# Performance work log

Hardware: AMD Instinct MI355X
Metric: run time of the kernel (lower is better)

The kernel has to match this reference:

```python
import jax, jax.numpy as jnp
import numpy as np


def _rel_index(h):
    # static relative-position index for an h x h grid (torch meshgrid 'ij')
    coords = np.stack(np.meshgrid(np.arange(h), np.arange(h), indexing='ij'))  # (2,h,h)
    cf = coords.reshape(2, -1)                       # (2, N)
    rel = cf[:, :, None] - cf[:, None, :]            # (2, N, N)
    rel = rel.transpose(1, 2, 0)                     # (N, N, 2)
    rel[..., 0] += h - 1
    rel[..., 1] += h - 1
    rel[..., 0] *= 2 * h - 1
    return rel.sum(-1)                               # (N, N) int


def _conv2d_s2(x, w, b):
    y = jax.lax.conv_general_dilated(x, w, window_strides=(2, 2),
                                     padding=[(1, 1), (1, 1)],
                                     dimension_numbers=('NCHW', 'OIHW', 'NCHW'))
    return y + b[None, :, None, None]


def _attn(z, qkv_w, qkv_b, out_w, out_b, table, heads):
    # H == reduce_size for every layer in this config, so no interp of K/V.
    B, C, H, W = z.shape
    N = H * W
    inner = qkv_w.shape[0] // 3
    d = inner // heads
    qkv = jnp.einsum('oc,bchw->bohw', qkv_w, z) + qkv_b[None, :, None, None]
    q, k, v = jnp.split(qkv, 3, axis=1)
    # channel layout is (dim_head, heads) with heads fastest (einops '(dim_head heads)')
    def split_heads(t):
        return t.reshape(B, d, heads, N).transpose(0, 2, 3, 1)  # b h n d
    q, k, v = split_heads(q), split_heads(k), split_heads(v)
    att = jnp.einsum('bhid,bhjd->bhij', q, k)
    idx = _rel_index(H)
    bias = table[idx.reshape(-1)].reshape(N, N, heads).transpose(2, 0, 1)  # (h, N, N)
    att = (att + bias[None]) * (d ** -0.5)  # bias added BEFORE scale, as in source
    att = jax.nn.softmax(att, axis=-1)
    o = jnp.einsum('bhij,bhjd->bhid', att, v)
    o = o.transpose(0, 3, 1, 2).reshape(B, d * heads, H, W)  # back to (dim_head heads) layout
    return jnp.einsum('oc,bchw->bohw', out_w, o) + out_b[None, :, None, None]


def setup_inputs() -> dict:
    key = jax.random.key(0)
    ks = jax.random.split(key, 24)
    heads = 3
    dims = [16, 32, 64]
    in_chs = [1, 16, 32]
    reds = [32, 16, 8]
    inp = {'x': jax.random.normal(ks[0], (32, 1, 64, 64), dtype=jnp.float32)}
    j = 1
    for i, (dim, cin, r) in enumerate(zip(dims, in_chs, reds), start=1):
        dh = dim // heads
        inner = dh * heads
        inp[f'conv{i}_w'] = jax.random.normal(ks[j], (dim, cin, 3, 3), dtype=jnp.float32) * 0.05; j += 1
        inp[f'conv{i}_b'] = jax.random.normal(ks[j], (dim,), dtype=jnp.float32) * 0.01; j += 1
        inp[f'qkv{i}_w'] = jax.random.normal(ks[j], (inner * 3, dim), dtype=jnp.float32) * 0.05; j += 1
        inp[f'qkv{i}_b'] = jax.random.normal(ks[j], (inner * 3,), dtype=jnp.float32) * 0.01; j += 1
        inp[f'out{i}_w'] = jax.random.normal(ks[j], (dim, inner), dtype=jnp.float32) * 0.05; j += 1
        inp[f'out{i}_b'] = jax.random.normal(ks[j], (dim,), dtype=jnp.float32) * 0.01; j += 1
        inp[f'rel{i}'] = jax.random.normal(ks[j], ((2 * r - 1) * (2 * r - 1), heads), dtype=jnp.float32) * 0.02; j += 1
    inp['cls_w'] = jax.random.normal(ks[j], (10, 64), dtype=jnp.float32) * 0.05; j += 1
    inp['cls_b'] = jax.random.normal(ks[j], (10,), dtype=jnp.float32) * 0.01
    return inp


def reference(x, conv1_w, conv1_b, qkv1_w, qkv1_b, out1_w, out1_b, rel1,
              conv2_w, conv2_b, qkv2_w, qkv2_b, out2_w, out2_b, rel2,
              conv3_w, conv3_b, qkv3_w, qkv3_b, out3_w, out3_b, rel3,
              cls_w, cls_b):
    heads = 3
    z = jax.nn.relu(_conv2d_s2(x, conv1_w, conv1_b))
    z = _attn(z, qkv1_w, qkv1_b, out1_w, out1_b, rel1, heads) + z
    z = jax.nn.relu(_conv2d_s2(z, conv2_w, conv2_b))
    z = _attn(z, qkv2_w, qkv2_b, out2_w, out2_b, rel2, heads) + z
    z = jax.nn.relu(_conv2d_s2(z, conv3_w, conv3_b))
    z = _attn(z, qkv3_w, qkv3_b, out3_w, out3_b, rel3, heads) + z
    z = z.mean(axis=(2, 3))           # adaptive avg pool to 1x1 + flatten -> (B, 64)
    cls_output = z @ cls_w.T + cls_b  # CLS_head linear (dropout inactive in eval)
    return (z, cls_output)
```

## Files before the change

kernel.cpp:

```cpp
#include <hip/hip_runtime.h>
#include <math.h>

#define CDIV(a, b) (((a) + (b) - 1) / (b))

#define LOG2E 1.4426950408889634f
#define SC5  (0.44721359549996f * LOG2E)
#define SC10 (0.31622776601684f * LOG2E)
#define SC21 (0.21821789023599f * LOG2E)
#define EXP2(x) __builtin_amdgcn_exp2f(x)

template <int CIN, int HIN, int COUT, int HOUT, int INNER, int DP, int KVRS, int KVD, int TPX>
__global__ void __launch_bounds__(256) conv_qkv(const float* __restrict__ in,
                                                const float* __restrict__ cw,
                                                const float* __restrict__ cb,
                                                const float* __restrict__ qw,
                                                const float* __restrict__ qb,
                                                float* __restrict__ z, float* __restrict__ q,
                                                float* __restrict__ kv) {
    constexpr int N = HOUT * HOUT;
    __shared__ float zt[COUT * TPX];
    const int b  = blockIdx.x / (N / TPX);
    const int n0 = (blockIdx.x % (N / TPX)) * TPX;
    const int tid = threadIdx.x;

    for (int idx = tid; idx < COUT * TPX; idx += 256) {
        int c = idx / TPX, px = idx % TPX;
        int n = n0 + px;
        int ho = n / HOUT, wo = n % HOUT;
        float acc = cb[c];
        for (int ci = 0; ci < CIN; ++ci) {
            const float* ip = in + (size_t)(b * CIN + ci) * HIN * HIN;
            const float* wp = cw + (size_t)(c * CIN + ci) * 9;
            #pragma unroll
            for (int kh = 0; kh < 3; ++kh) {
                int hi = 2 * ho + kh - 1;
                if (hi < 0 || hi >= HIN) continue;
                #pragma unroll
                for (int kw = 0; kw < 3; ++kw) {
                    int wi = 2 * wo + kw - 1;
                    if (wi < 0 || wi >= HIN) continue;
                    acc = fmaf(wp[kh * 3 + kw], ip[hi * HIN + wi], acc);
                }
            }
        }
        acc = fmaxf(acc, 0.f);
        zt[idx] = acc;
        z[((size_t)(b * COUT) + c) * N + n] = acc;
    }
    __syncthreads();

    constexpr int OC3 = 3 * INNER;
    for (int idx = tid; idx < OC3 * TPX; idx += 256) {
        int oc = idx / TPX, px = idx % TPX;
        float val = qb[oc];
        const float* wp = qw + (size_t)oc * COUT;
        #pragma unroll 8
        for (int c = 0; c < COUT; ++c) val = fmaf(wp[c], zt[c * TPX + px], val);
        int part = oc / INNER;
        int r = oc - part * INNER;
        int hh = r % 3, dd = r / 3;
        size_t n = n0 + px;
        if (part == 0)
            q[((size_t)(b * 3 + hh) * N + n) * DP + dd] = val;
        else
            kv[((size_t)(b * 3 + hh) * N + n) * KVRS + (part - 1) * KVD + dd] = val;
    }
}

template <int CPREV, int INNERP, int DPREV, int HINW, int COUT, int HOUT, int INNER, int DP,
          int KVRS, int KVD, int TPX>
__global__ void __launch_bounds__(256) fused_oc(const float* __restrict__ o1,
                                                const float* __restrict__ ow,
                                                const float* __restrict__ ob,
                                                const float* __restrict__ zres,
                                                const float* __restrict__ cw,
                                                const float* __restrict__ cb,
                                                const float* __restrict__ qw,
                                                const float* __restrict__ qb,
                                                float* __restrict__ z, float* __restrict__ q,
                                                float* __restrict__ kv) {
    constexpr int N2 = HOUT * HOUT;
    constexpr int N1 = HINW * HINW;
    constexpr int TROWS = TPX / HOUT;
    constexpr int HR = 2 * TROWS + 1;
    constexpr int HALO = HR * HINW;
    __shared__ float smem[INNERP * HALO + CPREV * HALO];
    float* o1s = smem;
    float* zh  = smem + INNERP * HALO;
    float* zt  = smem;
    const int b  = blockIdx.x / (N2 / TPX);
    const int n0 = (blockIdx.x % (N2 / TPX)) * TPX;
    const int tid = threadIdx.x;
    const int ho0 = n0 / HOUT;
    const int row0 = 2 * ho0 - 1;

    for (int t = tid; t < INNERP * HALO; t += 256) {
        int hd = t / HALO, p = t - hd * HALO;
        int row = row0 + p / HINW;
        float v = 0.f;
        if (row >= 0 && row < HINW)
            v = o1[((size_t)(b * INNERP + hd)) * N1 + row * HINW + (p % HINW)];
        o1s[t] = v;
    }
    __syncthreads();

    for (int t = tid; t < CPREV * HALO; t += 256) {
        int ci = t / HALO, p = t - ci * HALO;
        int row = row0 + p / HINW;
        float val = 0.f;
        if (row >= 0 && row < HINW) {
            int n1 = row * HINW + (p % HINW);
            val = ob[ci] + zres[((size_t)(b * CPREV) + ci) * N1 + n1];
            const float* wp = ow + (size_t)ci * INNERP;
            for (int dd = 0; dd < DPREV; ++dd) {
                #pragma unroll
                for (int hh = 0; hh < 3; ++hh)
                    val = fmaf(wp[dd * 3 + hh], o1s[(hh * DPREV + dd) * HALO + p], val);
            }
        }
        zh[t] = val;
    }
    __syncthreads();

    for (int idx = tid; idx < COUT * TPX; idx += 256) {
        int c = idx / TPX, px = idx - (idx / TPX) * TPX;
        int hol = px / HOUT, wo = px - hol * HOUT;
        float acc = cb[c];
        for (int ci = 0; ci < CPREV; ++ci) {
            const float* zp = zh + ci * HALO;
            const float* wp = cw + (size_t)(c * CPREV + ci) * 9;
            #pragma unroll
            for (int kh = 0; kh < 3; ++kh) {
                int r = 2 * hol + kh;
                #pragma unroll
                for (int kw = 0; kw < 3; ++kw) {
                    int col = 2 * wo + kw - 1;
                    if (col < 0 || col >= HINW) continue;
                    acc = fmaf(wp[kh * 3 + kw], zp[r * HINW + col], acc);
                }
            }
        }
        acc = fmaxf(acc, 0.f);
        zt[idx] = acc;
        z[((size_t)(b * COUT) + c) * N2 + n0 + px] = acc;
    }
    __syncthreads();

    constexpr int OC3 = 3 * INNER;
    for (int idx = tid; idx < OC3 * TPX; idx += 256) {
        int oc = idx / TPX, px = idx % TPX;
        float val = qb[oc];
        const float* wp = qw + (size_t)oc * COUT;
        #pragma unroll 8
        for (int c = 0; c < COUT; ++c) val = fmaf(wp[c], zt[c * TPX + px], val);
        int part = oc / INNER;
        int r = oc - part * INNER;
        int hh = r % 3, dd = r / 3;
        size_t n = n0 + px;
        if (part == 0)
            q[((size_t)(b * 3 + hh) * N2 + n) * DP + dd] = val;
        else
            kv[((size_t)(b * 3 + hh) * N2 + n) * KVRS + (part - 1) * KVD + dd] = val;
    }
}

template <int D, int QP, int RS, int RPT, int TILE, int NW>
__global__ void __launch_bounds__(NW * 64) attn_big(const float* __restrict__ q,
                                                    const float* __restrict__ kv,
                                                    const float* __restrict__ table,
                                                    float* __restrict__ o, int N, int log2Hg,
                                                    int T, float scale2) {
    extern __shared__ float smem[];
    float* tb = smem;
    float* comb = smem;
    constexpr int BT = NW * 64;
    constexpr int ROWS = 64 * RPT;
    constexpr int CSTR = (D % 2 == 0) ? (D + 3) : (D + 2);
    constexpr int RV4 = RS / 4;
    constexpr int NLD = (TILE * RV4 + 63) / 64;
    constexpr bool FULL = (TILE * RV4) % 64 == 0;

    const int bh = blockIdx.x % 96;
    const int chunk = blockIdx.x / 96;
    const int h = bh % 3;
    const int tid = threadIdx.x;
    const int wave = tid >> 6;
    const int lane = tid & 63;
    const int Hg = 1 << log2Hg;
    const int W2 = 2 * Hg - 1;
    const int base = chunk * ROWS;

    float* kvw = smem + ((T + 3) & ~3) + wave * (2 * TILE * RS);

    for (int t = tid; t < T; t += BT) tb[t] = table[t * 3 + h] * scale2;

    float qr[RPT][D];
    const float* tbp[RPT];
    #pragma unroll
    for (int r = 0; r < RPT; ++r) {
        int i = base + lane + 64 * r;
        const float* qg = q + ((size_t)bh * N + i) * QP;
        #pragma unroll
        for (int dd = 0; dd < D; ++dd) qr[r][dd] = qg[dd];
        tbp[r] = tb + (((i >> log2Hg) + Hg - 1) * W2 + (i & (Hg - 1)) + Hg - 1);
    }

    float acc[RPT][D];
    float lsum[RPT];
    #pragma unroll
    for (int r = 0; r < RPT; ++r) {
        lsum[r] = 0.f;
        #pragma unroll
        for (int dd = 0; dd < D; ++dd) acc[r][dd] = 0.f;
    }

    const float4* kvb4 = (const float4*)(kv + (size_t)bh * N * RS);
    const int NJ = N / NW;
    const int NT = NJ / TILE;
    const int j0 = wave * NJ;

    float4 sreg[NLD];
    {
        const float4* src = kvb4 + (size_t)j0 * RV4;
        #pragma unroll
        for (int x = 0; x < NLD; ++x) {
            int idx = lane + 64 * x;
            if (FULL || idx < TILE * RV4) sreg[x] = src[idx];
        }
        float4* dst4 = (float4*)kvw;
        #pragma unroll
        for (int x = 0; x < NLD; ++x) {
            int idx = lane + 64 * x;
            if (FULL || idx < TILE * RV4) dst4[idx] = sreg[x];
        }
    }

    __syncthreads();

    for (int t = 0; t < NT; ++t) {
        float* curb = kvw + (t & 1) * (TILE * RS);
        if (t + 1 < NT) {
            const float4* src = kvb4 + (size_t)(j0 + (t + 1) * TILE) * RV4;
            #pragma unroll
            for (int x = 0; x < NLD; ++x) {
                int idx = lane + 64 * x;
                if (FULL || idx < TILE * RV4) sreg[x] = src[idx];
            }
        }
        const int jt = j0 + t * TILE;
        for (int jg = 0; jg < TILE; jg += 4) {
            #pragma unroll
            for (int k = 0; k < 4; ++k) {
                const int j = jt + jg + k;
                const float* kr = curb + (jg + k) * RS;
                const int joff = (j >> log2Hg) * W2 + (j & (Hg - 1));
                #pragma unroll
                for (int r = 0; r < RPT; ++r) {
                    float s = 0.f;
                    #pragma unroll
                    for (int dd = 0; dd < D; ++dd) s = fmaf(qr[r][dd], kr[dd], s);
                    float e = EXP2(fmaf(s, scale2, tbp[r][-joff]));
                    lsum[r] += e;
                    #pragma unroll
                    for (int dd = 0; dd < D; ++dd) acc[r][dd] = fmaf(e, kr[D + dd], acc[r][dd]);
                }
            }
        }
        if (t + 1 < NT) {
            float4* dst4 = (float4*)(kvw + ((t + 1) & 1) * (TILE * RS));
            #pragma unroll
            for (int x = 0; x < NLD; ++x) {
                int idx = lane + 64 * x;
                if (FULL || idx < TILE * RV4) dst4[idx] = sreg[x];
            }
        }
    }

    __syncthreads();
    #pragma unroll
    for (int r = 0; r < RPT; ++r) {
        float* cp = comb + (size_t)(wave * ROWS + lane + 64 * r) * CSTR;
        #pragma unroll
        for (int dd = 0; dd < D; ++dd) cp[dd] = acc[r][dd];
        cp[D] = lsum[r];
    }
    __syncthreads();
    if (tid < ROWS) {
        float af[D];
        #pragma unroll
        for (int dd = 0; dd < D; ++dd) af[dd] = 0.f;
        float lf = 0.f;
        #pragma unroll
        for (int wv = 0; wv < NW; ++wv) {
            const float* cp = comb + (size_t)(wv * ROWS + tid) * CSTR;
            #pragma unroll
            for (int dd = 0; dd < D; ++dd) af[dd] += cp[dd];
            lf += cp[D];
        }
        float inv = 1.0f / lf;
        int i = base + tid;
        #pragma unroll
        for (int dd = 0; dd < D; ++dd)
            o[((size_t)bh * D + dd) * N + i] = af[dd] * inv;
    }
}

__global__ void __launch_bounds__(256) attn_small(const float* __restrict__ q,
                                                  const float* __restrict__ kv,
                                                  const float* __restrict__ table,
                                                  float* __restrict__ o, float scale2) {
    constexpr int D = 21, DP = 24, NN = 64;
    constexpr int CSTR = 23;
    __shared__ float smem[4 * NN * CSTR];
    float* kvs = smem;
    float* tb = kvs + NN * 2 * DP;
    float* comb = smem;

    const int bh = blockIdx.x;
    const int h = bh % 3;
    const int tid = threadIdx.x;
    const int wave = tid >> 6;
    const int lane = tid & 63;

    {
        const float4* kvg = (const float4*)(kv + (size_t)bh * NN * 2 * DP);
        float4* kvs4 = (float4*)kvs;
        for (int t = tid; t < NN * 2 * DP / 4; t += 256) kvs4[t] = kvg[t];
        for (int t = tid; t < 225; t += 256) tb[t] = table[t * 3 + h] * scale2;
    }

    const int i = lane;
    const float* qg = q + ((size_t)bh * NN + i) * DP;
    float qr[D];
    #pragma unroll
    for (int dd = 0; dd < D; ++dd) qr[dd] = qg[dd];
    const int ibase = ((i >> 3) + 7) * 15 + (i & 7) + 7;
    __syncthreads();

    float acc[D];
    #pragma unroll
    for (int dd = 0; dd < D; ++dd) acc[dd] = 0.f;
    float lsum = 0.f;

    const int j0 = wave * 16;
    #pragma unroll
    for (int jj = 0; jj < 16; ++jj) {
        const int j = j0 + jj;
        float4 r4[12];
        const float4* rp = (const float4*)(kvs + j * 2 * DP);
        #pragma unroll
        for (int x = 0; x < 12; ++x) r4[x] = rp[x];
        const float* kr = (const float*)r4;
        const float* vr = kr + DP;
        const int joff = (j >> 3) * 15 + (j & 7);
        float s = 0.f;
        #pragma unroll
        for (int dd = 0; dd < D; ++dd) s = fmaf(qr[dd], kr[dd], s);
        float e = EXP2(fmaf(s, scale2, tb[ibase - joff]));
        lsum += e;
        #pragma unroll
        for (int dd = 0; dd < D; ++dd) acc[dd] = fmaf(e, vr[dd], acc[dd]);
    }

    __syncthreads();
    {
        float* cp = comb + (size_t)(wave * NN + lane) * CSTR;
        #pragma unroll
        for (int dd = 0; dd < D; ++dd) cp[dd] = acc[dd];
        cp[D] = lsum;
    }
    __syncthreads();
    if (tid < NN) {
        float af[D];
        #pragma unroll
        for (int dd = 0; dd < D; ++dd) af[dd] = 0.f;
        float lf = 0.f;
        #pragma unroll
        for (int wv = 0; wv < 4; ++wv) {
            const float* cp = comb + (size_t)(wv * NN + tid) * CSTR;
            #pragma unroll
            for (int dd = 0; dd < D; ++dd) af[dd] += cp[dd];
            lf += cp[D];
        }
        float inv = 1.0f / lf;
        #pragma unroll
        for (int dd = 0; dd < D; ++dd)
            o[((size_t)bh * D + dd) * NN + tid] = af[dd] * inv;
    }
}

__global__ void __launch_bounds__(256) tail(const float* __restrict__ o,
                                            const float* __restrict__ ow,
                                            const float* __restrict__ ob,
                                            const float* __restrict__ zin,
                                            const float* __restrict__ cw,
                                            const float* __restrict__ cb,
                                            float* __restrict__ out) {
    __shared__ float os[63 * 64];
    __shared__ float zt[64 * 65];
    __shared__ float p[64];
    const int b = blockIdx.x;
    const int tid = threadIdx.x;
    for (int t = tid; t < 63 * 64; t += 256) os[t] = o[(size_t)(b * 63) * 64 + t];
    __syncthreads();
    for (int idx = tid; idx < 64 * 64; idx += 256) {
        int c = idx >> 6, n = idx & 63;
        float val = ob[c] + zin[((size_t)(b * 64) + c) * 64 + n];
        const float* wp = ow + (size_t)c * 63;
        for (int dd = 0; dd < 21; ++dd) {
            #pragma unroll
            for (int hh = 0; hh < 3; ++hh)
                val = fmaf(wp[dd * 3 + hh], os[(hh * 21 + dd) * 64 + n], val);
        }
        zt[c * 65 + n] = val;
    }
    __syncthreads();
    if (tid < 64) {
        float s = 0.f;
        #pragma unroll
        for (int n = 0; n < 64; ++n) s += zt[tid * 65 + n];
        s *= (1.0f / 64.0f);
        p[tid] = s;
        out[b * 64 + tid] = s;
    }
    __syncthreads();
    if (tid < 10) {
        float val = cb[tid];
        const float* wp = cw + (size_t)tid * 64;
        #pragma unroll
        for (int kk = 0; kk < 64; ++kk) val = fmaf(wp[kk], p[kk], val);
        out[2048 + b * 10 + tid] = val;
    }
}

extern "C" void kernel_launch(void* const* d_in, const int* in_sizes, int n_in,
                              void* d_out, int out_size, void* d_ws, size_t ws_size,
                              hipStream_t stream) {
    float* ws = (float*)d_ws;
    float* Zc1 = ws;
    float* Zc2 = Zc1 + 524288;
    float* Q   = Zc2 + 262144;
    float* KV  = Q + 786432;
    float* O   = KV + 1572864;

    float* out = (float*)d_out;

    conv_qkv<1, 64, 16, 32, 15, 8, 12, 5, 32><<<32 * 32, 256, 0, stream>>>(
        (const float*)d_in[0], (const float*)d_in[1], (const float*)d_in[2],
        (const float*)d_in[3], (const float*)d_in[4], Zc1, Q, KV);
    attn_big<5, 8, 12, 2, 64, 4><<<96 * 8, 256, 40464, stream>>>(
        Q, KV, (const float*)d_in[7], O, 1024, 5, 3969, SC5);

    fused_oc<16, 15, 5, 32, 32, 16, 30, 12, 20, 10, 16><<<32 * 16, 256, 0, stream>>>(
        O, (const float*)d_in[5], (const float*)d_in[6], Zc1,
        (const float*)d_in[8], (const float*)d_in[9],
        (const float*)d_in[10], (const float*)d_in[11], Zc2, Q, KV);
    attn_big<10, 12, 20, 1, 32, 8><<<96 * 4, 512, 44816, stream>>>(
        Q, KV, (const float*)d_in[14], O, 256, 4, 961, SC10);

    fused_oc<32, 30, 10, 16, 64, 8, 63, 24, 48, 24, 8><<<32 * 8, 256, 0, stream>>>(
        O, (const float*)d_in[12], (const float*)d_in[13], Zc2,
        (const float*)d_in[15], (const float*)d_in[16],
        (const float*)d_in[17], (const float*)d_in[18], Zc1, Q, KV);
    attn_small<<<96, 256, 0, stream>>>(Q, KV, (const float*)d_in[21], O, SC21);

    tail<<<32, 256, 0, stream>>>(
        O, (const float*)d_in[19], (const float*)d_in[20], Zc1,
        (const float*)d_in[22], (const float*)d_in[23], out);
}
```

Before: 277.9 us.

## Stage attention K/V tiles via direct global-to-LDS loads with two-tile lookahead

Replaces the register-staged double buffering of K/V tiles in attn_big with __builtin_amdgcn_global_load_lds, which writes global data straight into LDS, and issues two tiles ahead, synchronising with explicit vmcnt/lgkmcnt waits. The aim is to free registers and hide global load latency across more compute. Correctness relies on hand-placed waitcnt literals that assume exactly three loads per tile, and on the first tile being complete before the initial barrier. Nothing is added to wait on the vector-memory counter before that barrier, so tile 0 may not have landed in LDS when compute starts.

```diff
diff --git a/kernel.cpp b/kernel.cpp
--- a/kernel.cpp
+++ b/kernel.cpp
@@ -8,6 +8,15 @@
 #define SC10 (0.31622776601684f * LOG2E)
 #define SC21 (0.21821789023599f * LOG2E)
 #define EXP2(x) __builtin_amdgcn_exp2f(x)
+
+template <int N> __device__ inline void waitcnt_vm() {
+    if constexpr (N == 0) asm volatile("s_waitcnt vmcnt(0)" ::: "memory");
+    else if constexpr (N == 2) asm volatile("s_waitcnt vmcnt(2)" ::: "memory");
+    else if constexpr (N == 3) asm volatile("s_waitcnt vmcnt(3)" ::: "memory");
+    else if constexpr (N == 4) asm volatile("s_waitcnt vmcnt(4)" ::: "memory");
+    else if constexpr (N == 6) asm volatile("s_waitcnt vmcnt(6)" ::: "memory");
+    else static_assert(N < 0, "unsupported vmcnt literal");
+}
 
 template <int CIN, int HIN, int COUT, int HOUT, int INNER, int DP, int KVRS, int KVD, int TPX>
 __global__ void __launch_bounds__(256) conv_qkv(const float* __restrict__ in,
@@ -177,8 +186,10 @@
     constexpr int ROWS = 64 * RPT;
     constexpr int CSTR = (D % 2 == 0) ? (D + 3) : (D + 2);
     constexpr int RV4 = RS / 4;
-    constexpr int NLD = (TILE * RV4 + 63) / 64;
-    constexpr bool FULL = (TILE * RV4) % 64 == 0;
+    constexpr int TBYTES = TILE * RS * 4;
+    constexpr int LPT = CDIV(TBYTES, 1024);
+    constexpr bool FULLT = (TBYTES % 1024) == 0;
+    static_assert(LPT == 3, "vmcnt literal below assumes 3 loads per tile");
 
     const int bh = blockIdx.x % 96;
     const int chunk = blockIdx.x / 96;
@@ -214,39 +225,33 @@
         for (int dd = 0; dd < D; ++dd) acc[r][dd] = 0.f;
     }
 
-    const float4* kvb4 = (const float4*)(kv + (size_t)bh * N * RS);
+    const float* kvbase = kv + (size_t)bh * N * RS;
     const int NJ = N / NW;
     const int NT = NJ / TILE;
     const int j0 = wave * NJ;
 
-    float4 sreg[NLD];
-    {
-        const float4* src = kvb4 + (size_t)j0 * RV4;
-        #pragma unroll
-        for (int x = 0; x < NLD; ++x) {
-            int idx = lane + 64 * x;
-            if (FULL || idx < TILE * RV4) sreg[x] = src[idx];
-        }
-        float4* dst4 = (float4*)kvw;
-        #pragma unroll
-        for (int x = 0; x < NLD; ++x) {
-            int idx = lane + 64 * x;
-            if (FULL || idx < TILE * RV4) dst4[idx] = sreg[x];
-        }
-    }
+    auto stage = [&](int bufIdx, int t) {
+        const float* srcf = kvbase + (size_t)(j0 + t * TILE) * RS;
+        float* dstf = kvw + bufIdx * (TILE * RS);
+        #pragma unroll
+        for (int x = 0; x < LPT; ++x) {
+            if (FULLT || (x * 1024 + lane * 16) < TBYTES) {
+                const void* g = (const void*)(srcf + x * 256 + lane * 4);
+                void* l = (void*)(dstf + x * 256);
+                __builtin_amdgcn_global_load_lds(
+                    (const __attribute__((address_space(1))) void*)g,
+                    (__attribute__((address_space(3))) void*)l, 16, 0, 0);
+            }
+        }
+    };
+
+    stage(0, 0);
+    if (NT > 1) stage(1, 1);
 
     __syncthreads();
 
     for (int t = 0; t < NT; ++t) {
-        float* curb = kvw + (t & 1) * (TILE * RS);
-        if (t + 1 < NT) {
-            const float4* src = kvb4 + (size_t)(j0 + (t + 1) * TILE) * RV4;
-            #pragma unroll
-            for (int x = 0; x < NLD; ++x) {
-                int idx = lane + 64 * x;
-                if (FULL || idx < TILE * RV4) sreg[x] = src[idx];
-            }
-        }
+        const float* curb = kvw + (t & 1) * (TILE * RS);
         const int jt = j0 + t * TILE;
         for (int jg = 0; jg < TILE; jg += 4) {
             #pragma unroll
@@ -266,13 +271,12 @@
                 }
             }
         }
-        if (t + 1 < NT) {
-            float4* dst4 = (float4*)(kvw + ((t + 1) & 1) * (TILE * RS));
-            #pragma unroll
-            for (int x = 0; x < NLD; ++x) {
-                int idx = lane + 64 * x;
-                if (FULL || idx < TILE * RV4) dst4[idx] = sreg[x];
-            }
+        if (t + 2 < NT) {
+            asm volatile("s_waitcnt lgkmcnt(0)" ::: "memory");
+            stage(t & 1, t + 2);
+            waitcnt_vm<3>();
+        } else if (t + 1 < NT) {
+            waitcnt_vm<0>();
         }
     }
 
```

Result: no change. 278.4 us (+0.2%).
